# Performance work log

Hardware: AMD Instinct MI355X
Metric: run time of the kernel (lower is better)

## Reference

```python
import jax, jax.numpy as jnp
import numpy as np

N_CLUSTER = 5      # prototypes per class (init arg n_cluster)
NUM_CLASSES = 6    # hard-coded by `i // (len(prototypes)//6)` in the torch source


def setup_inputs() -> dict:
    key = jax.random.key(0)
    k0, k1, k2, k3 = jax.random.split(key, 4)
    B, C, H, W = 8, 256, 128, 128
    P = NUM_CLASSES * N_CLUSTER  # 30
    return {
        "assp_features": jax.random.normal(k0, (B, C, H, W), jnp.float32),
        "prototypes": jax.random.normal(k1, (P, B, C), jnp.float32),
        # key 1x1 conv == linear over channels: weight [128, C], bias [128]
        "Wk": jax.random.normal(k2, (128, C), jnp.float32) * 0.05,
        "bk": jnp.zeros((128,), jnp.float32),
        # one query 1x1 conv per class: [num_classes, 128, C] / [num_classes, 128]
        "Wq": jax.random.normal(k3, (NUM_CLASSES, 128, C), jnp.float32) * 0.05,
        "bq": jnp.zeros((NUM_CLASSES, 128), jnp.float32),
    }


def reference(assp_features, prototypes, Wk, bk, Wq, bq):
    B, C, H, W = assp_features.shape
    P = prototypes.shape[0]
    G = P // NUM_CLASSES  # prototypes sharing each class query

    # key: 1x1 conv -> [B, 128, H*W]
    key_out = jnp.einsum('bchw,kc->bkhw', assp_features, Wk) + bk[None, :, None, None]
    key_flat = key_out.reshape(B, 128, H * W)

    # queries: prototype i uses query_{i // G}; batch all P projections at once
    proto_g = prototypes.reshape(NUM_CLASSES, G, B, C)
    q = jnp.einsum('gpbc,gkc->gpbk', proto_g, Wq) + bq[:, None, None, :]
    q = q.reshape(P, B, 128)  # prototypesOut stacked: [P, B, 128]

    # similarity: bmm([B,1,128],[B,128,HW]) per prototype -> [B, P, H, W]
    sim = jnp.einsum('pbk,bkn->bpn', q, key_flat).reshape(B, P, H, W)

    # softmax(sim / P * n_cluster) over prototype axis, then max over prototypes
    w = jax.nn.softmax(sim * (N_CLUSTER / P), axis=1)
    w = jnp.max(w, axis=1)  # [B, H, W]

    assp_weighted = assp_features * w[:, None, :, :]
    return (assp_weighted, q, sim)
```

## Files before the change

kernel.cpp:

```cpp
#include <hip/hip_runtime.h>

#define BB    8
#define CC    256
#define HWN   16384
#define PP    30
#define PPAD  32
#define KD    128
#define GG    5
#define XsS   34
#define OFF_Q   (33554432u)
#define OFF_SIM (OFF_Q + 30720u)

typedef float  f32x4 __attribute__((ext_vector_type(4)));
typedef short  short8 __attribute__((ext_vector_type(8)));

static __device__ __forceinline__ unsigned short f2bf(float f) {
    unsigned u = __float_as_uint(f);
    u += 0x7fffu + ((u >> 16) & 1u);
    return (unsigned short)(u >> 16);
}

__global__ __launch_bounds__(256) void proj_kernel(
    const float* __restrict__ proto,
    const float* __restrict__ Wq,
    const float* __restrict__ bq,
    const float* __restrict__ Wk,
    const float* __restrict__ bk,
    float* __restrict__ qout,
    short* __restrict__ Afrag,
    float* __restrict__ c0)
{
    const int pb = blockIdx.x;
    const int p = pb / BB, b = pb % BB;
    const int tid = threadIdx.x;

    const int kb = tid >> 5, sub = (tid >> 3) & 3, j = tid & 7;
    const int lane = (p & 15) + 16 * sub;
    const size_t fidx = (((size_t)(b * 2 + (p >> 4)) * 8 + kb) * 64 + lane) * 8 + j;

    if (p >= PP) {
        Afrag[fidx] = 0;
        if (tid == 0) c0[b * PPAD + p] = -1e30f;
        return;
    }
    const int g = p / GG;

    __shared__ float ps[CC];
    __shared__ float qs[KD];

    for (int c = tid; c < CC; c += 256)
        ps[c] = proto[(size_t)(p * BB + b) * CC + c];
    __syncthreads();

    if (tid < KD) {
        const float* wrow = Wq + (size_t)(g * KD + tid) * CC;
        float a = 0.f;
        #pragma unroll 4
        for (int c = 0; c < CC; ++c) a += ps[c] * wrow[c];
        a += bq[g * KD + tid];
        qout[(size_t)(p * BB + b) * KD + tid] = a;
        qs[tid] = a;
    }
    __syncthreads();

    float a = 0.f;
    #pragma unroll 4
    for (int k = 0; k < KD; ++k) a += qs[k] * Wk[k * CC + tid];
    Afrag[fidx] = (short)f2bf(a);

    if (tid == 0) {
        float s = 0.f;
        for (int k = 0; k < KD; ++k) s += qs[k] * bk[k];
        c0[b * PPAD + p] = s;
    }
}

__global__ __launch_bounds__(128, 4) void fused_kernel(
    const float* __restrict__ X,
    const short* __restrict__ Afrag,
    const float* __restrict__ c0,
    float* __restrict__ out0,
    float* __restrict__ sim)
{
    const int b    = blockIdx.y;
    const int tid  = threadIdx.x;
    const int lane = tid & 63;
    const int w    = tid >> 6;
    const int col  = lane & 15;
    const int kgrp = lane >> 4;
    const int n0   = blockIdx.x * 32;
    const int nw   = n0 + w * 16;

    __shared__ unsigned short Xs[CC * XsS];
    __shared__ float c0s[PPAD];
    __shared__ float wbuf[32];

    if (tid < PPAD) c0s[tid] = c0[b * PPAD + tid];

    const short8* af8 = (const short8*)Afrag;
    const size_t afbase = (size_t)b * 2 * 8 * 64;
    short8 afA[8], afB[8];
    #pragma unroll
    for (int kb = 0; kb < 8; ++kb) {
        afA[kb] = af8[afbase + (size_t)kb * 64 + lane];
        afB[kb] = af8[afbase + (size_t)(8 + kb) * 64 + lane];
    }

    const int ch_s = tid >> 3;
    const int pq_s = tid & 7;
    {
        const float* gb = X + (size_t)b * CC * HWN + n0;
        #pragma unroll
        for (int it = 0; it < 4; ++it) {
            f32x4 v[4];
            #pragma unroll
            for (int u = 0; u < 4; ++u) {
                const int ch = (it * 4 + u) * 16 + ch_s;
                v[u] = *(const f32x4*)(gb + (size_t)ch * HWN + pq_s * 4);
            }
            #pragma unroll
            for (int u = 0; u < 4; ++u) {
                const int ch = (it * 4 + u) * 16 + ch_s;
                const unsigned lo = (unsigned)f2bf(v[u].x) | ((unsigned)f2bf(v[u].y) << 16);
                const unsigned hi = (unsigned)f2bf(v[u].z) | ((unsigned)f2bf(v[u].w) << 16);
                unsigned* dst = (unsigned*)&Xs[ch * XsS + pq_s * 4];
                dst[0] = lo;
                dst[1] = hi;
            }
        }
    }
    __syncthreads();

    f32x4 accA = {}, accB = {};
    #pragma unroll
    for (int kb = 0; kb < 8; ++kb) {
        short8 bfr;
        #pragma unroll
        for (int j = 0; j < 8; ++j)
            bfr[j] = (short)Xs[(kb * 32 + kgrp * 8 + j) * XsS + w * 16 + col];
        accA = __builtin_amdgcn_mfma_f32_16x16x32_bf16(afA[kb], bfr, accA, 0, 0, 0);
        accB = __builtin_amdgcn_mfma_f32_16x16x32_bf16(afB[kb], bfr, accB, 0, 0, 0);
    }

    float v[8];
    float pm = -1e30f;
    #pragma unroll
    for (int r = 0; r < 4; ++r) {
        const int row = kgrp * 4 + r;
        const float tA = accA[r] + c0s[row];
        const float tB = accB[r] + c0s[row + 16];
        v[r] = tA;
        v[r + 4] = tB;
        pm = fmaxf(pm, fmaxf(tA, tB));
        __builtin_nontemporal_store(tA,
            sim + ((size_t)b * PP + row) * HWN + nw + col);
        if (row + 16 < PP)
            __builtin_nontemporal_store(tB,
                sim + ((size_t)b * PP + row + 16) * HWN + nw + col);
    }
    float m = pm;
    m = fmaxf(m, __shfl_xor(m, 16));
    m = fmaxf(m, __shfl_xor(m, 32));

    float s = 0.f;
    #pragma unroll
    for (int r = 0; r < 8; ++r)
        s += __expf((v[r] - m) * (1.f / 6.f));
    s += __shfl_xor(s, 16);
    s += __shfl_xor(s, 32);

    if (lane < 16) wbuf[w * 16 + lane] = 1.f / s;
    __syncthreads();

    const f32x4 w4 = *(const f32x4*)(&wbuf[pq_s * 4]);
    float* ob = out0 + (size_t)b * CC * HWN + n0 + pq_s * 4;
    #pragma unroll 4
    for (int i = 0; i < 16; ++i) {
        const int ch = ch_s * 16 + i;
        const unsigned* src = (const unsigned*)&Xs[ch * XsS + pq_s * 4];
        const unsigned lo = src[0], hi = src[1];
        f32x4 x;
        x.x = __uint_as_float(lo << 16);
        x.y = __uint_as_float(lo & 0xffff0000u);
        x.z = __uint_as_float(hi << 16);
        x.w = __uint_as_float(hi & 0xffff0000u);
        __builtin_nontemporal_store(x * w4, (f32x4*)(ob + (size_t)ch * HWN));
    }
}

extern "C" void kernel_launch(void* const* d_in, const int* in_sizes, int n_in,
                              void* d_out, int out_size, void* d_ws, size_t ws_size,
                              hipStream_t stream) {
    const float* X     = (const float*)d_in[0];
    const float* proto = (const float*)d_in[1];
    const float* Wk    = (const float*)d_in[2];
    const float* bk    = (const float*)d_in[3];
    const float* Wq    = (const float*)d_in[4];
    const float* bq    = (const float*)d_in[5];

    float* out  = (float*)d_out;
    float* qout = out + OFF_Q;
    float* sim  = out + OFF_SIM;

    short* Afrag = (short*)d_ws;
    float* c0    = (float*)(Afrag + BB * 2 * 8 * 64 * 8);

    proj_kernel<<<PPAD * BB, 256, 0, stream>>>(proto, Wq, bq, Wk, bk, qout, Afrag, c0);

    dim3 grid(HWN / 32, BB);
    fused_kernel<<<grid, 128, 0, stream>>>(X, Afrag, c0, out, sim);
}
```

Before: 67.58 us.

## Keep full-precision X tile in registers and store weighted output from them

The fused kernel now holds all 16 loaded float4 X vectors in registers, issuing every global load up front instead of in groups of four. The weighted output is computed from these fp32 registers rather than from the bf16 tile in shared memory. This removes the LDS read-back and restores full precision in the first output. The A fragments are now loaded per k-block inside the MFMA loop rather than preloaded, and the occupancy hint is dropped from launch bounds. Holding 64 extra floats live across the MFMA phase raises register pressure and may reduce occupancy.

```diff
diff --git a/kernel.cpp b/kernel.cpp
--- a/kernel.cpp
+++ b/kernel.cpp
@@ -75,7 +75,7 @@
     }
 }
 
-__global__ __launch_bounds__(128, 4) void fused_kernel(
+__global__ __launch_bounds__(128) void fused_kernel(
     const float* __restrict__ X,
     const short* __restrict__ Afrag,
     const float* __restrict__ c0,
@@ -97,49 +97,40 @@
 
     if (tid < PPAD) c0s[tid] = c0[b * PPAD + tid];
 
-    const short8* af8 = (const short8*)Afrag;
-    const size_t afbase = (size_t)b * 2 * 8 * 64;
-    short8 afA[8], afB[8];
-    #pragma unroll
-    for (int kb = 0; kb < 8; ++kb) {
-        afA[kb] = af8[afbase + (size_t)kb * 64 + lane];
-        afB[kb] = af8[afbase + (size_t)(8 + kb) * 64 + lane];
-    }
-
     const int ch_s = tid >> 3;
     const int pq_s = tid & 7;
+    f32x4 L[16];
     {
         const float* gb = X + (size_t)b * CC * HWN + n0;
         #pragma unroll
-        for (int it = 0; it < 4; ++it) {
-            f32x4 v[4];
-            #pragma unroll
-            for (int u = 0; u < 4; ++u) {
-                const int ch = (it * 4 + u) * 16 + ch_s;
-                v[u] = *(const f32x4*)(gb + (size_t)ch * HWN + pq_s * 4);
-            }
-            #pragma unroll
-            for (int u = 0; u < 4; ++u) {
-                const int ch = (it * 4 + u) * 16 + ch_s;
-                const unsigned lo = (unsigned)f2bf(v[u].x) | ((unsigned)f2bf(v[u].y) << 16);
-                const unsigned hi = (unsigned)f2bf(v[u].z) | ((unsigned)f2bf(v[u].w) << 16);
-                unsigned* dst = (unsigned*)&Xs[ch * XsS + pq_s * 4];
-                dst[0] = lo;
-                dst[1] = hi;
-            }
-        }
+        for (int it = 0; it < 16; ++it)
+            L[it] = *(const f32x4*)(gb + (size_t)(it * 16 + ch_s) * HWN + pq_s * 4);
+    }
+    #pragma unroll
+    for (int it = 0; it < 16; ++it) {
+        const int ch = it * 16 + ch_s;
+        const unsigned lo = (unsigned)f2bf(L[it].x) | ((unsigned)f2bf(L[it].y) << 16);
+        const unsigned hi = (unsigned)f2bf(L[it].z) | ((unsigned)f2bf(L[it].w) << 16);
+        unsigned* dst = (unsigned*)&Xs[ch * XsS + pq_s * 4];
+        dst[0] = lo;
+        dst[1] = hi;
     }
     __syncthreads();
+
+    const short8* af8 = (const short8*)Afrag;
+    const size_t afbase = (size_t)b * 2 * 8 * 64;
 
     f32x4 accA = {}, accB = {};
     #pragma unroll
     for (int kb = 0; kb < 8; ++kb) {
+        const short8 afA = af8[afbase + (size_t)kb * 64 + lane];
+        const short8 afB = af8[afbase + (size_t)(8 + kb) * 64 + lane];
         short8 bfr;
         #pragma unroll
         for (int j = 0; j < 8; ++j)
             bfr[j] = (short)Xs[(kb * 32 + kgrp * 8 + j) * XsS + w * 16 + col];
-        accA = __builtin_amdgcn_mfma_f32_16x16x32_bf16(afA[kb], bfr, accA, 0, 0, 0);
-        accB = __builtin_amdgcn_mfma_f32_16x16x32_bf16(afB[kb], bfr, accB, 0, 0, 0);
+        accA = __builtin_amdgcn_mfma_f32_16x16x32_bf16(afA, bfr, accA, 0, 0, 0);
+        accB = __builtin_amdgcn_mfma_f32_16x16x32_bf16(afB, bfr, accB, 0, 0, 0);
     }
 
     float v[8];
@@ -174,17 +165,10 @@
 
     const f32x4 w4 = *(const f32x4*)(&wbuf[pq_s * 4]);
     float* ob = out0 + (size_t)b * CC * HWN + n0 + pq_s * 4;
-    #pragma unroll 4
-    for (int i = 0; i < 16; ++i) {
-        const int ch = ch_s * 16 + i;
-        const unsigned* src = (const unsigned*)&Xs[ch * XsS + pq_s * 4];
-        const unsigned lo = src[0], hi = src[1];
-        f32x4 x;
-        x.x = __uint_as_float(lo << 16);
-        x.y = __uint_as_float(lo & 0xffff0000u);
-        x.z = __uint_as_float(hi << 16);
-        x.w = __uint_as_float(hi & 0xffff0000u);
-        __builtin_nontemporal_store(x * w4, (f32x4*)(ob + (size_t)ch * HWN));
+    #pragma unroll
+    for (int it = 0; it < 16; ++it) {
+        const int ch = it * 16 + ch_s;
+        __builtin_nontemporal_store(L[it] * w4, (f32x4*)(ob + (size_t)ch * HWN));
     }
 }
 
```

Result: slower. 70.69 us (+4.6%).

## Split fused kernel into sim/weight kernel and separate scaling pass

Applied to the files above, without the earlier changes.

Breaks the fused kernel in two. The first kernel computes sim and a per-pixel softmax-max weight and writes that weight to workspace. A separate streaming kernel then re-reads X in fp32 and writes X times the weight. A-fragments are now loaded per k-step instead of being held in registers, and the occupancy hint is dropped, reducing register pressure. This adds a full second read of X (128MB) but makes the output exact fp32 rather than bf16-rounded X.

```diff
diff --git a/kernel.cpp b/kernel.cpp
--- a/kernel.cpp
+++ b/kernel.cpp
@@ -75,11 +75,11 @@
     }
 }
 
-__global__ __launch_bounds__(128, 4) void fused_kernel(
+__global__ __launch_bounds__(128) void sim_kernel(
     const float* __restrict__ X,
     const short* __restrict__ Afrag,
     const float* __restrict__ c0,
-    float* __restrict__ out0,
+    float* __restrict__ wq,
     float* __restrict__ sim)
 {
     const int b    = blockIdx.y;
@@ -93,18 +93,8 @@
 
     __shared__ unsigned short Xs[CC * XsS];
     __shared__ float c0s[PPAD];
-    __shared__ float wbuf[32];
 
     if (tid < PPAD) c0s[tid] = c0[b * PPAD + tid];
-
-    const short8* af8 = (const short8*)Afrag;
-    const size_t afbase = (size_t)b * 2 * 8 * 64;
-    short8 afA[8], afB[8];
-    #pragma unroll
-    for (int kb = 0; kb < 8; ++kb) {
-        afA[kb] = af8[afbase + (size_t)kb * 64 + lane];
-        afB[kb] = af8[afbase + (size_t)(8 + kb) * 64 + lane];
-    }
 
     const int ch_s = tid >> 3;
     const int pq_s = tid & 7;
@@ -131,15 +121,20 @@
     }
     __syncthreads();
 
+    const short8* af8 = (const short8*)Afrag;
+    const size_t afbase = (size_t)b * 2 * 8 * 64;
+
     f32x4 accA = {}, accB = {};
     #pragma unroll
     for (int kb = 0; kb < 8; ++kb) {
+        const short8 afA = af8[afbase + (size_t)kb * 64 + lane];
+        const short8 afB = af8[afbase + (size_t)(8 + kb) * 64 + lane];
         short8 bfr;
         #pragma unroll
         for (int j = 0; j < 8; ++j)
             bfr[j] = (short)Xs[(kb * 32 + kgrp * 8 + j) * XsS + w * 16 + col];
-        accA = __builtin_amdgcn_mfma_f32_16x16x32_bf16(afA[kb], bfr, accA, 0, 0, 0);
-        accB = __builtin_amdgcn_mfma_f32_16x16x32_bf16(afB[kb], bfr, accB, 0, 0, 0);
+        accA = __builtin_amdgcn_mfma_f32_16x16x32_bf16(afA, bfr, accA, 0, 0, 0);
+        accB = __builtin_amdgcn_mfma_f32_16x16x32_bf16(afB, bfr, accB, 0, 0, 0);
     }
 
     float v[8];
@@ -169,22 +164,28 @@
     s += __shfl_xor(s, 16);
     s += __shfl_xor(s, 32);
 
-    if (lane < 16) wbuf[w * 16 + lane] = 1.f / s;
-    __syncthreads();
-
-    const f32x4 w4 = *(const f32x4*)(&wbuf[pq_s * 4]);
-    float* ob = out0 + (size_t)b * CC * HWN + n0 + pq_s * 4;
-    #pragma unroll 4
-    for (int i = 0; i < 16; ++i) {
-        const int ch = ch_s * 16 + i;
-        const unsigned* src = (const unsigned*)&Xs[ch * XsS + pq_s * 4];
-        const unsigned lo = src[0], hi = src[1];
-        f32x4 x;
-        x.x = __uint_as_float(lo << 16);
-        x.y = __uint_as_float(lo & 0xffff0000u);
-        x.z = __uint_as_float(hi << 16);
-        x.w = __uint_as_float(hi & 0xffff0000u);
-        __builtin_nontemporal_store(x * w4, (f32x4*)(ob + (size_t)ch * HWN));
+    if (lane < 16)
+        wq[(size_t)b * HWN + nw + lane] = 1.f / s;
+}
+
+__global__ __launch_bounds__(256) void scale_kernel(
+    const float* __restrict__ X,
+    const float* __restrict__ wq,
+    float* __restrict__ out0)
+{
+    const unsigned t = blockIdx.x * 256 + threadIdx.x;
+    const f32x4* X4 = (const f32x4*)X;
+    const f32x4* W4 = (const f32x4*)wq;
+    f32x4*       O4 = (f32x4*)out0;
+
+    #pragma unroll
+    for (int k = 0; k < 16; ++k) {
+        const unsigned i  = t + ((unsigned)k << 19);
+        const unsigned b  = i >> 20;
+        const unsigned n4 = i & 4095;
+        const f32x4 x = X4[i];
+        const f32x4 w = W4[(b << 12) + n4];
+        __builtin_nontemporal_store(x * w, &O4[i]);
     }
 }
 
@@ -204,9 +205,12 @@
 
     short* Afrag = (short*)d_ws;
     float* c0    = (float*)(Afrag + BB * 2 * 8 * 64 * 8);
+    float* wq    = c0 + BB * PPAD;
 
     proj_kernel<<<PPAD * BB, 256, 0, stream>>>(proto, Wq, bq, Wk, bk, qout, Afrag, c0);
 
     dim3 grid(HWN / 32, BB);
-    fused_kernel<<<grid, 128, 0, stream>>>(X, Afrag, c0, out, sim);
-}
+    sim_kernel<<<grid, 128, 0, stream>>>(X, Afrag, c0, wq, sim);
+
+    scale_kernel<<<2048, 256, 0, stream>>>(X, wq, out);
+}
```

Result: slower. 93.62 us (+38.5%).
